# Kernel optimization log

Hardware: AMD Instinct MI355X
Metric: run time of the kernel (lower is better)

## Reference

```python
import jax, jax.numpy as jnp
import numpy as np

NQ = 8          # n_qubits
NC = 4          # n_cycles of the angle encoder
PI = np.float32(np.pi)
LAYER_QUBITS = [[0, 1, 2, 3, 4, 5, 6, 7], [1, 3, 5, 7]]  # active qubits per conv layer
FINAL_QUBITS = [3, 7]                                    # active after last pooling
CX = jnp.array([[1, 0, 0, 0], [0, 1, 0, 0], [0, 0, 0, 1], [0, 0, 1, 0]], jnp.complex64)


def apply1(psi, U, q):
    """Apply 1-qubit gate U ((2,2) shared or (B,2,2) batched) on qubit q. psi: (B,2,...,2)."""
    psi = jnp.moveaxis(psi, 1 + q, -1)
    if U.ndim == 3:
        psi = jnp.einsum('bij,b...j->b...i', U, psi)
    else:
        psi = jnp.einsum('ij,...j->...i', U, psi)
    return jnp.moveaxis(psi, -1, 1 + q)


def apply2(psi, U, q0, q1):
    """Apply 2-qubit gate U (4,4) on (q0,q1); q0 is the more-significant wire."""
    psi = jnp.moveaxis(psi, (1 + q0, 1 + q1), (-2, -1))
    sh = psi.shape
    psi = jnp.einsum('ij,...j->...i', U, psi.reshape(sh[:-2] + (4,)))
    return jnp.moveaxis(psi.reshape(sh), (-2, -1), (1 + q0, 1 + q1))


def rz_mat(t):
    return jnp.array([[jnp.exp(-0.5j * t), 0.0], [0.0, jnp.exp(0.5j * t)]]).astype(jnp.complex64)


def ry_mat(t):
    c, s = jnp.cos(t / 2), jnp.sin(t / 2)
    return jnp.array([[c, -s], [s, c]]).astype(jnp.complex64)


def crx_mat(t):
    c = jnp.cos(t / 2).astype(jnp.complex64)
    s = jnp.sin(t / 2).astype(jnp.complex64)
    M = jnp.eye(4, dtype=jnp.complex64)
    return M.at[2, 2].set(c).at[3, 3].set(c).at[2, 3].set(-1j * s).at[3, 2].set(-1j * s)


def u3_mat(t, p, l):
    c, s = jnp.cos(t / 2), jnp.sin(t / 2)
    return jnp.array([[c + 0j, -jnp.exp(1j * l) * s],
                      [jnp.exp(1j * p) * s, jnp.exp(1j * (p + l)) * c]]).astype(jnp.complex64)


def expz(psi, q):
    """<Z_q> = P(q=0) - P(q=1)."""
    p = psi.real ** 2 + psi.imag ** 2
    p = jnp.moveaxis(p, 1 + q, 1).reshape(p.shape[0], 2, -1).sum(-1)
    return p[:, 0] - p[:, 1]


def encode(x):
    """Angle-encoding circuit (circuit_builder): NC cycles of RY(x) + CNOT ring."""
    B = x.shape[0]
    psi = jnp.zeros((B, 2 ** NQ), jnp.complex64).at[:, 0].set(1.0).reshape((B,) + (2,) * NQ)
    for c in range(NC):
        ang = x[:, c * NQ:(c + 1) * NQ]
        cc, ss = jnp.cos(ang / 2), jnp.sin(ang / 2)
        for q in range(NQ):
            U = jnp.stack([jnp.stack([cc[:, q], -ss[:, q]], -1),
                           jnp.stack([ss[:, q], cc[:, q]], -1)], -2).astype(jnp.complex64)
            psi = apply1(psi, U, q)
        for q in range(NQ):
            psi = apply2(psi, CX, q, (q + 1) % NQ)
    return psi


def forward(x, rz_p, ry_p, ry2_p, crx_p, u3_p, u3b_p, W1, b1, W2, b2):
    psi0 = encode(x)
    psi1 = psi0  # deepcopy of encoded state for the second feature map
    for layer in range(2):
        aq = LAYER_QUBITS[layer]
        n = len(aq)
        RZp, RYp, RY2p = rz_mat(rz_p[layer]), ry_mat(ry_p[layer]), ry_mat(ry2_p[layer])
        RZm, RZpl = rz_mat(-PI / 2), rz_mat(PI / 2)
        # circuit 1: ZNOTY-style conv blocks, even pairs then odd pairs
        for parity in (0, 1):
            for i in range(parity, n - 1, 2):
                qc, qt = aq[i], aq[i + 1]
                psi0 = apply1(psi0, RZm, qt)
                psi0 = apply2(psi0, CX, qt, qc)
                psi0 = apply1(psi0, RZp, qc)
                psi0 = apply1(psi0, RYp, qt)
                psi0 = apply2(psi0, CX, qc, qt)
                psi0 = apply1(psi0, RY2p, qt)
                psi0 = apply2(psi0, CX, qt, qc)
                psi0 = apply1(psi0, RZpl, qc)
        remain = [aq[i] for i in range(n) if i % 2 == 1]
        U3a = u3_mat(u3_p[layer, 0], u3_p[layer, 1], u3_p[layer, 2])
        for q in remain:
            psi0 = apply1(psi0, U3a, q)
        # circuit 2: CRX conv blocks, even pairs then odd pairs
        CRXp = crx_mat(crx_p[layer])
        for parity in (0, 1):
            for i in range(parity, n - 1, 2):
                psi1 = apply2(psi1, CRXp, aq[i], aq[i + 1])
        U3b = u3_mat(u3b_p[layer, 0], u3b_p[layer, 1], u3b_p[layer, 2])
        for q in remain:
            psi1 = apply1(psi1, U3b, q)
    xv = jnp.stack([expz(psi0, q) for q in FINAL_QUBITS], 1)  # (B,2)
    yv = jnp.stack([expz(psi1, q) for q in FINAL_QUBITS], 1)  # (B,2)
    feat = jnp.concatenate([xv, yv], 1)                       # (B,4)
    h = jnp.tanh(feat @ W1.T + b1)
    return jax.nn.sigmoid(h @ W2.T + b2)


def setup_inputs() -> dict:
    key = jax.random.key(0)
    ks = jax.random.split(key, 12)
    B = 8192
    return {
        'x': jax.random.normal(ks[0], (B, NC * NQ), jnp.float32),
        'rz_p': jax.random.normal(ks[1], (2,), jnp.float32) * 0.5,
        'ry_p': jax.random.normal(ks[2], (2,), jnp.float32) * 0.5,
        'ry2_p': jax.random.normal(ks[3], (2,), jnp.float32) * 0.5,
        'crx_p': jax.random.normal(ks[4], (2,), jnp.float32) * 0.5,
        'u3_p': jax.random.normal(ks[5], (2, 3), jnp.float32) * 0.5,
        'u3b_p': jax.random.normal(ks[6], (2, 3), jnp.float32) * 0.5,
        'W1': jax.random.normal(ks[7], (15, 4), jnp.float32) * 0.4,
        'b1': jax.random.normal(ks[8], (15,), jnp.float32) * 0.1,
        'W2': jax.random.normal(ks[9], (1, 15), jnp.float32) * 0.25,
        'b2': jax.random.normal(ks[10], (1,), jnp.float32) * 0.1,
    }


def reference(x, rz_p, ry_p, ry2_p, crx_p, u3_p, u3b_p, W1, b1, W2, b2):
    return forward(x, rz_p, ry_p, ry2_p, crx_p, u3_p, u3b_p, W1, b1, W2, b2)
```

## Files before the change

kernel.cpp:

```cpp
#include <hip/hip_runtime.h>

#define DEV __device__ __forceinline__

struct C2 { float r, i; };


template<int P>
DEV void ry_cross(float* pr, float* pi, float gc, float gs, int lane) {
  const float cb = ((lane >> P) & 1) ? gs : -gs;
  #pragma unroll
  for (int s = 0; s < 16; ++s) {
    float br = __shfl_xor(pr[s], 1 << P);
    float bi = __shfl_xor(pi[s], 1 << P);
    pr[s] = gc * pr[s] + cb * br;
    pi[s] = gc * pi[s] + cb * bi;
  }
}

template<int M>
DEV void ry_in(float* pr, float* pi, float gc, float gs) {
  #pragma unroll
  for (int s = 0; s < 16; ++s) if (!(s & M)) {
    const int s1 = s | M;
    float ar = pr[s], ai = pi[s], br = pr[s1], bi = pi[s1];
    pr[s]  = gc * ar - gs * br;  pi[s]  = gc * ai - gs * bi;
    pr[s1] = gs * ar + gc * br;  pi[s1] = gs * ai + gc * bi;
  }
}

template<int PC, int PT>
DEV void cx_cc(float* pr, float* pi, int lane) {
  const bool h = (lane >> PC) & 1;
  #pragma unroll
  for (int s = 0; s < 16; ++s) {
    float tr = __shfl_xor(pr[s], 1 << PT);
    float ti = __shfl_xor(pi[s], 1 << PT);
    pr[s] = h ? tr : pr[s];
    pi[s] = h ? ti : pi[s];
  }
}

template<int PC, int MT>
DEV void cx_ci(float* pr, float* pi, int lane) {
  const bool h = (lane >> PC) & 1;
  #pragma unroll
  for (int s = 0; s < 16; ++s) if (!(s & MT)) {
    const int s1 = s | MT;
    float ar = pr[s], br = pr[s1];
    pr[s] = h ? br : ar;  pr[s1] = h ? ar : br;
    float ai = pi[s], bi = pi[s1];
    pi[s] = h ? bi : ai;  pi[s1] = h ? ai : bi;
  }
}

template<int MC, int MT>
DEV void cx_ii(float* pr, float* pi) {
  #pragma unroll
  for (int s = 0; s < 16; ++s) if ((s & MC) && !(s & MT)) {
    const int s1 = s | MT;
    float t;
    t = pr[s]; pr[s] = pr[s1]; pr[s1] = t;
    t = pi[s]; pi[s] = pi[s1]; pi[s1] = t;
  }
}

template<int MC, int PT>
DEV void cx_ic(float* pr, float* pi) {
  #pragma unroll
  for (int s = 0; s < 16; ++s) if (s & MC) {
    pr[s] = __shfl_xor(pr[s], 1 << PT);
    pi[s] = __shfl_xor(pi[s], 1 << PT);
  }
}


template<int PC, int PT>
DEV void u4_cc(float* pr, float* pi, const float* cw, int lay, int lane) {
  const int bc = (lane >> PC) & 1, bt = (lane >> PT) & 1;
  const int r = (bc << 1) | bt;
  const int base = (lay * 16 + r * 4) * 2;
  const float w0r = cw[base + (r ^ 0) * 2], w0i = cw[base + (r ^ 0) * 2 + 1];
  const float w1r = cw[base + (r ^ 1) * 2], w1i = cw[base + (r ^ 1) * 2 + 1];
  const float w2r = cw[base + (r ^ 2) * 2], w2i = cw[base + (r ^ 2) * 2 + 1];
  const float w3r = cw[base + (r ^ 3) * 2], w3i = cw[base + (r ^ 3) * 2 + 1];
  #pragma unroll
  for (int s = 0; s < 16; ++s) {
    float ar = pr[s], ai = pi[s];
    float tr = __shfl_xor(ar, 1 << PT), ti = __shfl_xor(ai, 1 << PT);
    float cr = __shfl_xor(ar, 1 << PC), ci = __shfl_xor(ai, 1 << PC);
    float ur = __shfl_xor(tr, 1 << PC), ui = __shfl_xor(ti, 1 << PC);
    pr[s] = w0r*ar - w0i*ai + w1r*tr - w1i*ti + w2r*cr - w2i*ci + w3r*ur - w3i*ui;
    pi[s] = w0r*ai + w0i*ar + w1r*ti + w1i*tr + w2r*ci + w2i*cr + w3r*ui + w3i*ur;
  }
}

template<int PC, int MT>
DEV void u4_ci(float* pr, float* pi, const float* cw, int lay, int lane) {
  const int bc = (lane >> PC) & 1;
  const int r0 = bc << 1, r1 = r0 | 1;
  const int b0 = (lay * 16 + r0 * 4) * 2;
  const int b1 = (lay * 16 + r1 * 4) * 2;
  const float A0r = cw[b0 + (r0 ^ 0) * 2], A0i = cw[b0 + (r0 ^ 0) * 2 + 1];
  const float A1r = cw[b0 + (r0 ^ 1) * 2], A1i = cw[b0 + (r0 ^ 1) * 2 + 1];
  const float A2r = cw[b0 + (r0 ^ 2) * 2], A2i = cw[b0 + (r0 ^ 2) * 2 + 1];
  const float A3r = cw[b0 + (r0 ^ 3) * 2], A3i = cw[b0 + (r0 ^ 3) * 2 + 1];
  const float B0r = cw[b1 + (r1 ^ 0) * 2], B0i = cw[b1 + (r1 ^ 0) * 2 + 1];
  const float B1r = cw[b1 + (r1 ^ 1) * 2], B1i = cw[b1 + (r1 ^ 1) * 2 + 1];
  const float B2r = cw[b1 + (r1 ^ 2) * 2], B2i = cw[b1 + (r1 ^ 2) * 2 + 1];
  const float B3r = cw[b1 + (r1 ^ 3) * 2], B3i = cw[b1 + (r1 ^ 3) * 2 + 1];
  #pragma unroll
  for (int s = 0; s < 16; ++s) if (!(s & MT)) {
    const int s1 = s | MT;
    float ar = pr[s], ai = pi[s], br = pr[s1], bi = pi[s1];
    float xar = __shfl_xor(ar, 1 << PC), xai = __shfl_xor(ai, 1 << PC);
    float xbr = __shfl_xor(br, 1 << PC), xbi = __shfl_xor(bi, 1 << PC);
    pr[s]  = A0r*ar - A0i*ai + A1r*br - A1i*bi + A2r*xar - A2i*xai + A3r*xbr - A3i*xbi;
    pi[s]  = A0r*ai + A0i*ar + A1r*bi + A1i*br + A2r*xai + A2i*xar + A3r*xbi + A3i*xbr;
    pr[s1] = B0r*br - B0i*bi + B1r*ar - B1i*ai + B2r*xbr - B2i*xbi + B3r*xar - B3i*xai;
    pi[s1] = B0r*bi + B0i*br + B1r*ai + B1i*ar + B2r*xbi + B2i*xbr + B3r*xai + B3i*xar;
  }
}

template<int MC, int MT>
DEV void u4_ii(float* pr, float* pi, const float* cw, int lay) {
  float u[32];
  #pragma unroll
  for (int k = 0; k < 32; ++k) u[k] = cw[lay * 32 + k];
  #pragma unroll
  for (int s = 0; s < 16; ++s) if (!(s & (MC | MT))) {
    const int s0 = s, s1 = s | MT, s2 = s | MC, s3 = s | MC | MT;
    float v0r = pr[s0], v0i = pi[s0], v1r = pr[s1], v1i = pi[s1];
    float v2r = pr[s2], v2i = pi[s2], v3r = pr[s3], v3i = pi[s3];
    float n0r = u[0]*v0r - u[1]*v0i + u[2]*v1r - u[3]*v1i + u[4]*v2r - u[5]*v2i + u[6]*v3r - u[7]*v3i;
    float n0i = u[0]*v0i + u[1]*v0r + u[2]*v1i + u[3]*v1r + u[4]*v2i + u[5]*v2r + u[6]*v3i + u[7]*v3r;
    float n1r = u[8]*v0r - u[9]*v0i + u[10]*v1r - u[11]*v1i + u[12]*v2r - u[13]*v2i + u[14]*v3r - u[15]*v3i;
    float n1i = u[8]*v0i + u[9]*v0r + u[10]*v1i + u[11]*v1r + u[12]*v2i + u[13]*v2r + u[14]*v3i + u[15]*v3r;
    float n2r = u[16]*v0r - u[17]*v0i + u[18]*v1r - u[19]*v1i + u[20]*v2r - u[21]*v2i + u[22]*v3r - u[23]*v3i;
    float n2i = u[16]*v0i + u[17]*v0r + u[18]*v1i + u[19]*v1r + u[20]*v2i + u[21]*v2r + u[22]*v3i + u[23]*v3r;
    float n3r = u[24]*v0r - u[25]*v0i + u[26]*v1r - u[27]*v1i + u[28]*v2r - u[29]*v2i + u[30]*v3r - u[31]*v3i;
    float n3i = u[24]*v0i + u[25]*v0r + u[26]*v1i + u[27]*v1r + u[28]*v2i + u[29]*v2r + u[30]*v3i + u[31]*v3r;
    pr[s0] = n0r; pi[s0] = n0i; pr[s1] = n1r; pi[s1] = n1i;
    pr[s2] = n2r; pi[s2] = n2i; pr[s3] = n3r; pi[s3] = n3i;
  }
}


DEV void u3_make(float t, float p, float l, C2* u) {
  float c = __cosf(0.5f * t), s = __sinf(0.5f * t);
  float cp = __cosf(p), sp = __sinf(p);
  float cl = __cosf(l), sl = __sinf(l);
  float cpl = __cosf(p + l), spl = __sinf(p + l);
  u[0] = C2{c, 0.0f};
  u[1] = C2{-cl * s, -sl * s};
  u[2] = C2{cp * s, sp * s};
  u[3] = C2{cpl * c, spl * c};
}

template<int P>
DEV void u3_cross(float* pr, float* pi, const C2* u, int lane) {
  const bool h = (lane >> P) & 1;
  const float car = h ? u[3].r : u[0].r, cai = h ? u[3].i : u[0].i;
  const float cbr = h ? u[2].r : u[1].r, cbi = h ? u[2].i : u[1].i;
  #pragma unroll
  for (int s = 0; s < 16; ++s) {
    float br = __shfl_xor(pr[s], 1 << P);
    float bi = __shfl_xor(pi[s], 1 << P);
    float ar = pr[s], ai = pi[s];
    pr[s] = car*ar - cai*ai + cbr*br - cbi*bi;
    pi[s] = car*ai + cai*ar + cbr*bi + cbi*br;
  }
}

template<int M>
DEV void u3_in(float* pr, float* pi, const C2* u) {
  #pragma unroll
  for (int s = 0; s < 16; ++s) if (!(s & M)) {
    const int s1 = s | M;
    float ar = pr[s], ai = pi[s], br = pr[s1], bi = pi[s1];
    pr[s]  = u[0].r*ar - u[0].i*ai + u[1].r*br - u[1].i*bi;
    pi[s]  = u[0].r*ai + u[0].i*ar + u[1].r*bi + u[1].i*br;
    pr[s1] = u[2].r*ar - u[2].i*ai + u[3].r*br - u[3].i*bi;
    pi[s1] = u[2].r*ai + u[2].i*ar + u[3].r*bi + u[3].i*br;
  }
}


template<int PC, int PT>
DEV void crx_cc(float* pr, float* pi, float c, float s, int lane) {
  const bool h = (lane >> PC) & 1;
  const float cc = h ? c : 1.0f;
  const float ss = h ? s : 0.0f;
  #pragma unroll
  for (int k = 0; k < 16; ++k) {
    float br = __shfl_xor(pr[k], 1 << PT);
    float bi = __shfl_xor(pi[k], 1 << PT);
    float ar = pr[k], ai = pi[k];
    pr[k] = cc * ar + ss * bi;
    pi[k] = cc * ai - ss * br;
  }
}

template<int PC, int MT>
DEV void crx_ci(float* pr, float* pi, float c, float s, int lane) {
  const bool h = (lane >> PC) & 1;
  const float cc = h ? c : 1.0f;
  const float ss = h ? s : 0.0f;
  #pragma unroll
  for (int k = 0; k < 16; ++k) if (!(k & MT)) {
    const int k1 = k | MT;
    float ar = pr[k], ai = pi[k], br = pr[k1], bi = pi[k1];
    pr[k]  = cc * ar + ss * bi;
    pi[k]  = cc * ai - ss * br;
    pr[k1] = cc * br + ss * ai;
    pi[k1] = cc * bi - ss * ar;
  }
}

template<int MC, int MT>
DEV void crx_ii(float* pr, float* pi, float c, float s) {
  #pragma unroll
  for (int k = 0; k < 16; ++k) if ((k & MC) && !(k & MT)) {
    const int k1 = k | MT;
    float ar = pr[k], ai = pi[k], br = pr[k1], bi = pi[k1];
    pr[k]  = c * ar + s * bi;
    pi[k]  = c * ai - s * br;
    pr[k1] = c * br + s * ai;
    pi[k1] = c * bi - s * ar;
  }
}


DEV void expz37(const float* pr, const float* pi, int lane, float& z3, float& z7) {
  float t3 = 0.0f, t7 = 0.0f;
  #pragma unroll
  for (int s = 0; s < 16; ++s) {
    float p = pr[s] * pr[s] + pi[s] * pi[s];
    t3 += p;
    t7 += (s & 1) ? -p : p;
  }
  t3 = (lane & 1) ? -t3 : t3;
  #pragma unroll
  for (int m = 1; m < 16; m <<= 1) {
    t3 += __shfl_xor(t3, m);
    t7 += __shfl_xor(t7, m);
  }
  z3 = t3; z7 = t7;
}


__global__ __launch_bounds__(256, 2)
void qcnn_kernel(const float* __restrict__ x,
                 const float* __restrict__ rz_p, const float* __restrict__ ry_p,
                 const float* __restrict__ ry2_p, const float* __restrict__ crx_p,
                 const float* __restrict__ u3_p, const float* __restrict__ u3b_p,
                 const float* __restrict__ W1, const float* __restrict__ b1,
                 const float* __restrict__ W2, const float* __restrict__ b2,
                 float* __restrict__ out, int B) {
  __shared__ float cw[64];

  const int tid  = threadIdx.x;
  const int lane = tid & 63;
  const int wave = tid >> 6;
  const int grp  = lane >> 4;
  const int sub  = lane & 15;
  const int elem = blockIdx.x * 16 + wave * 4 + grp;
  const int elemc = elem < B ? elem : (B - 1);

  if (lane < 32) {
    const int lay = lane >> 4, e = lane & 15, i4 = e >> 2, j4 = e & 3;
    const int base = lane & 48;
    const float c45 = 0.70710678118654752f;
    float rz = rz_p[lay], ry = ry_p[lay], ry2 = ry2_p[lay];
    float mr = (i4 == j4) ? c45 : 0.0f;
    float mi = (i4 == j4) ? ((i4 & 1) ? -c45 : c45) : 0.0f;
    { int t = (i4 & 1) ? (i4 ^ 2) : i4; int src = base | (t << 2) | j4;
      mr = __shfl(mr, src); mi = __shfl(mi, src); }
    { float cz = __cosf(0.5f * rz), sz = __sinf(0.5f * rz);
      float di = (i4 & 2) ? sz : -sz;
      float nr = cz * mr - di * mi, ni = cz * mi + di * mr; mr = nr; mi = ni; }
    { float cy = __cosf(0.5f * ry), sy = __sinf(0.5f * ry);
      int src = base | ((i4 ^ 1) << 2) | j4;
      float orr = __shfl(mr, src), oii = __shfl(mi, src);
      float sg = (i4 & 1) ? sy : -sy;
      mr = cy * mr + sg * orr; mi = cy * mi + sg * oii; }
    { int t = (i4 & 2) ? (i4 ^ 1) : i4; int src = base | (t << 2) | j4;
      mr = __shfl(mr, src); mi = __shfl(mi, src); }
    { float cy = __cosf(0.5f * ry2), sy = __sinf(0.5f * ry2);
      int src = base | ((i4 ^ 1) << 2) | j4;
      float orr = __shfl(mr, src), oii = __shfl(mi, src);
      float sg = (i4 & 1) ? sy : -sy;
      mr = cy * mr + sg * orr; mi = cy * mi + sg * oii; }
    { int t = (i4 & 1) ? (i4 ^ 2) : i4; int src = base | (t << 2) | j4;
      mr = __shfl(mr, src); mi = __shfl(mi, src); }
    { float di = (i4 & 2) ? c45 : -c45;
      float nr = c45 * mr - di * mi, ni = c45 * mi + di * mr; mr = nr; mi = ni; }
    cw[(lay * 16 + e) * 2]     = mr;
    cw[(lay * 16 + e) * 2 + 1] = mi;
  }

  float2 aa = ((const float2*)x)[(size_t)elemc * 16 + sub];
  float ch0 = __cosf(0.5f * aa.x), sh0 = __sinf(0.5f * aa.x);
  float ch1 = __cosf(0.5f * aa.y), sh1 = __sinf(0.5f * aa.y);

  float pr[16], pi[16];
  #pragma unroll
  for (int s = 0; s < 16; ++s) { pr[s] = 0.0f; pi[s] = 0.0f; }
  pr[0] = (sub == 0) ? 1.0f : 0.0f;

  #pragma unroll 1
  for (int c = 0; c < 4; ++c) {
    const int sb = lane & 48;
    float gc, gs;
    gc = __shfl(ch0, sb | (c * 4 + 0)); gs = __shfl(sh0, sb | (c * 4 + 0));
    ry_cross<3>(pr, pi, gc, gs, lane);
    gc = __shfl(ch1, sb | (c * 4 + 0)); gs = __shfl(sh1, sb | (c * 4 + 0));
    ry_cross<2>(pr, pi, gc, gs, lane);
    gc = __shfl(ch0, sb | (c * 4 + 1)); gs = __shfl(sh0, sb | (c * 4 + 1));
    ry_cross<1>(pr, pi, gc, gs, lane);
    gc = __shfl(ch1, sb | (c * 4 + 1)); gs = __shfl(sh1, sb | (c * 4 + 1));
    ry_cross<0>(pr, pi, gc, gs, lane);
    gc = __shfl(ch0, sb | (c * 4 + 2)); gs = __shfl(sh0, sb | (c * 4 + 2));
    ry_in<8>(pr, pi, gc, gs);
    gc = __shfl(ch1, sb | (c * 4 + 2)); gs = __shfl(sh1, sb | (c * 4 + 2));
    ry_in<4>(pr, pi, gc, gs);
    gc = __shfl(ch0, sb | (c * 4 + 3)); gs = __shfl(sh0, sb | (c * 4 + 3));
    ry_in<2>(pr, pi, gc, gs);
    gc = __shfl(ch1, sb | (c * 4 + 3)); gs = __shfl(sh1, sb | (c * 4 + 3));
    ry_in<1>(pr, pi, gc, gs);
    cx_cc<3, 2>(pr, pi, lane);
    cx_cc<2, 1>(pr, pi, lane);
    cx_cc<1, 0>(pr, pi, lane);
    cx_ci<0, 8>(pr, pi, lane);
    cx_ii<8, 4>(pr, pi);
    cx_ii<4, 2>(pr, pi);
    cx_ii<2, 1>(pr, pi);
    cx_ic<1, 3>(pr, pi);
  }

  float qr[16], qi[16];
  #pragma unroll
  for (int s = 0; s < 16; ++s) { qr[s] = pr[s]; qi[s] = pi[s]; }

  __syncthreads();

  u4_cc<3, 2>(pr, pi, cw, 0, lane);
  u4_cc<1, 0>(pr, pi, cw, 0, lane);
  u4_ii<8, 4>(pr, pi, cw, 0);
  u4_ii<2, 1>(pr, pi, cw, 0);
  u4_cc<2, 1>(pr, pi, cw, 0, lane);
  u4_ci<0, 8>(pr, pi, cw, 0, lane);
  u4_ii<4, 2>(pr, pi, cw, 0);
  {
    C2 u[4]; u3_make(u3_p[0], u3_p[1], u3_p[2], u);
    u3_cross<2>(pr, pi, u, lane);
    u3_cross<0>(pr, pi, u, lane);
    u3_in<4>(pr, pi, u);
    u3_in<1>(pr, pi, u);
  }
  u4_cc<2, 0>(pr, pi, cw, 1, lane);
  u4_ii<4, 1>(pr, pi, cw, 1);
  u4_ci<0, 4>(pr, pi, cw, 1, lane);
  {
    C2 u[4]; u3_make(u3_p[3], u3_p[4], u3_p[5], u);
    u3_cross<0>(pr, pi, u, lane);
    u3_in<1>(pr, pi, u);
  }

  {
    float t = crx_p[0];
    float cc = __cosf(0.5f * t), ss = __sinf(0.5f * t);
    crx_cc<3, 2>(qr, qi, cc, ss, lane);
    crx_cc<1, 0>(qr, qi, cc, ss, lane);
    crx_ii<8, 4>(qr, qi, cc, ss);
    crx_ii<2, 1>(qr, qi, cc, ss);
    crx_cc<2, 1>(qr, qi, cc, ss, lane);
    crx_ci<0, 8>(qr, qi, cc, ss, lane);
    crx_ii<4, 2>(qr, qi, cc, ss);
  }
  {
    C2 u[4]; u3_make(u3b_p[0], u3b_p[1], u3b_p[2], u);
    u3_cross<2>(qr, qi, u, lane);
    u3_cross<0>(qr, qi, u, lane);
    u3_in<4>(qr, qi, u);
    u3_in<1>(qr, qi, u);
  }
  {
    float t = crx_p[1];
    float cc = __cosf(0.5f * t), ss = __sinf(0.5f * t);
    crx_cc<2, 0>(qr, qi, cc, ss, lane);
    crx_ii<4, 1>(qr, qi, cc, ss);
    crx_ci<0, 4>(qr, qi, cc, ss, lane);
  }
  {
    C2 u[4]; u3_make(u3b_p[3], u3b_p[4], u3b_p[5], u);
    u3_cross<0>(qr, qi, u, lane);
    u3_in<1>(qr, qi, u);
  }

  float f0, f1, f2, f3;
  expz37(pr, pi, lane, f0, f1);
  expz37(qr, qi, lane, f2, f3);

  const int j = (sub < 15) ? sub : 0;
  float acc = W1[j * 4 + 0] * f0 + W1[j * 4 + 1] * f1 +
              W1[j * 4 + 2] * f2 + W1[j * 4 + 3] * f3 + b1[j];
  float e2 = __expf(2.0f * acc);
  float th = (e2 - 1.0f) / (e2 + 1.0f);
  float part = (sub < 15) ? th * W2[j] : 0.0f;
  #pragma unroll
  for (int m = 1; m < 16; m <<= 1) part += __shfl_xor(part, m);

  if (sub == 0 && elem < B) {
    float z = part + b2[0];
    out[elem] = 1.0f / (1.0f + __expf(-z));
  }
}

extern "C" void kernel_launch(void* const* d_in, const int* in_sizes, int n_in,
                              void* d_out, int out_size, void* d_ws, size_t ws_size,
                              hipStream_t stream) {
  (void)n_in; (void)out_size; (void)d_ws; (void)ws_size;
  const float* x     = (const float*)d_in[0];
  const float* rz_p  = (const float*)d_in[1];
  const float* ry_p  = (const float*)d_in[2];
  const float* ry2_p = (const float*)d_in[3];
  const float* crx_p = (const float*)d_in[4];
  const float* u3_p  = (const float*)d_in[5];
  const float* u3b_p = (const float*)d_in[6];
  const float* W1    = (const float*)d_in[7];
  const float* b1    = (const float*)d_in[8];
  const float* W2    = (const float*)d_in[9];
  const float* b2    = (const float*)d_in[10];
  float* out = (float*)d_out;

  const int B = in_sizes[0] / 32;
  const int blocks = (B + 15) / 16;
  qcnn_kernel<<<dim3(blocks), dim3(256), 0, stream>>>(
      x, rz_p, ry_p, ry2_p, crx_p, u3_p, u3b_p, W1, b1, W2, b2, out, B);
}
```

Measured before the change: 133.1 us.

## Map each batch element's 256-amplitude state to a full wavefront

Each state vector is now spread across a full 64-lane wave with 4 amplitudes per lane, instead of 16 lanes with 16 amplitudes each. All gate helpers are remapped so most qubits become cross-lane shuffles, and a dense 4x4 in-register gate is added. Blocks now handle 4 elements instead of 16, and the launch bound asks for more resident blocks. The aim is to cut register pressure and raise occupancy, at the cost of many more cross-lane shuffles per gate.

```diff
diff --git a/kernel.cpp b/kernel.cpp
--- a/kernel.cpp
+++ b/kernel.cpp
@@ -9,7 +9,7 @@
 DEV void ry_cross(float* pr, float* pi, float gc, float gs, int lane) {
   const float cb = ((lane >> P) & 1) ? gs : -gs;
   #pragma unroll
-  for (int s = 0; s < 16; ++s) {
+  for (int s = 0; s < 4; ++s) {
     float br = __shfl_xor(pr[s], 1 << P);
     float bi = __shfl_xor(pi[s], 1 << P);
     pr[s] = gc * pr[s] + cb * br;
@@ -20,7 +20,7 @@
 template<int M>
 DEV void ry_in(float* pr, float* pi, float gc, float gs) {
   #pragma unroll
-  for (int s = 0; s < 16; ++s) if (!(s & M)) {
+  for (int s = 0; s < 4; ++s) if (!(s & M)) {
     const int s1 = s | M;
     float ar = pr[s], ai = pi[s], br = pr[s1], bi = pi[s1];
     pr[s]  = gc * ar - gs * br;  pi[s]  = gc * ai - gs * bi;
@@ -32,7 +32,7 @@
 DEV void cx_cc(float* pr, float* pi, int lane) {
   const bool h = (lane >> PC) & 1;
   #pragma unroll
-  for (int s = 0; s < 16; ++s) {
+  for (int s = 0; s < 4; ++s) {
     float tr = __shfl_xor(pr[s], 1 << PT);
     float ti = __shfl_xor(pi[s], 1 << PT);
     pr[s] = h ? tr : pr[s];
@@ -44,7 +44,7 @@
 DEV void cx_ci(float* pr, float* pi, int lane) {
   const bool h = (lane >> PC) & 1;
   #pragma unroll
-  for (int s = 0; s < 16; ++s) if (!(s & MT)) {
+  for (int s = 0; s < 4; ++s) if (!(s & MT)) {
     const int s1 = s | MT;
     float ar = pr[s], br = pr[s1];
     pr[s] = h ? br : ar;  pr[s1] = h ? ar : br;
@@ -56,7 +56,7 @@
 template<int MC, int MT>
 DEV void cx_ii(float* pr, float* pi) {
   #pragma unroll
-  for (int s = 0; s < 16; ++s) if ((s & MC) && !(s & MT)) {
+  for (int s = 0; s < 4; ++s) if ((s & MC) && !(s & MT)) {
     const int s1 = s | MT;
     float t;
     t = pr[s]; pr[s] = pr[s1]; pr[s1] = t;
@@ -67,7 +67,7 @@
 template<int MC, int PT>
 DEV void cx_ic(float* pr, float* pi) {
   #pragma unroll
-  for (int s = 0; s < 16; ++s) if (s & MC) {
+  for (int s = 0; s < 4; ++s) if (s & MC) {
     pr[s] = __shfl_xor(pr[s], 1 << PT);
     pi[s] = __shfl_xor(pi[s], 1 << PT);
   }
@@ -76,19 +76,18 @@
 
 template<int PC, int PT>
 DEV void u4_cc(float* pr, float* pi, const float* cw, int lay, int lane) {
-  const int bc = (lane >> PC) & 1, bt = (lane >> PT) & 1;
-  const int r = (bc << 1) | bt;
+  const int r = (((lane >> PC) & 1) << 1) | ((lane >> PT) & 1);
   const int base = (lay * 16 + r * 4) * 2;
   const float w0r = cw[base + (r ^ 0) * 2], w0i = cw[base + (r ^ 0) * 2 + 1];
   const float w1r = cw[base + (r ^ 1) * 2], w1i = cw[base + (r ^ 1) * 2 + 1];
   const float w2r = cw[base + (r ^ 2) * 2], w2i = cw[base + (r ^ 2) * 2 + 1];
   const float w3r = cw[base + (r ^ 3) * 2], w3i = cw[base + (r ^ 3) * 2 + 1];
   #pragma unroll
-  for (int s = 0; s < 16; ++s) {
+  for (int s = 0; s < 4; ++s) {
     float ar = pr[s], ai = pi[s];
-    float tr = __shfl_xor(ar, 1 << PT), ti = __shfl_xor(ai, 1 << PT);
-    float cr = __shfl_xor(ar, 1 << PC), ci = __shfl_xor(ai, 1 << PC);
-    float ur = __shfl_xor(tr, 1 << PC), ui = __shfl_xor(ti, 1 << PC);
+    float tr = __shfl_xor(ar, 1 << PT),              ti = __shfl_xor(ai, 1 << PT);
+    float cr = __shfl_xor(ar, 1 << PC),              ci = __shfl_xor(ai, 1 << PC);
+    float ur = __shfl_xor(ar, (1 << PC) | (1 << PT)), ui = __shfl_xor(ai, (1 << PC) | (1 << PT));
     pr[s] = w0r*ar - w0i*ai + w1r*tr - w1i*ti + w2r*cr - w2i*ci + w3r*ur - w3i*ui;
     pi[s] = w0r*ai + w0i*ar + w1r*ti + w1i*tr + w2r*ci + w2i*cr + w3r*ui + w3i*ur;
   }
@@ -109,7 +108,7 @@
   const float B2r = cw[b1 + (r1 ^ 2) * 2], B2i = cw[b1 + (r1 ^ 2) * 2 + 1];
   const float B3r = cw[b1 + (r1 ^ 3) * 2], B3i = cw[b1 + (r1 ^ 3) * 2 + 1];
   #pragma unroll
-  for (int s = 0; s < 16; ++s) if (!(s & MT)) {
+  for (int s = 0; s < 4; ++s) if (!(s & MT)) {
     const int s1 = s | MT;
     float ar = pr[s], ai = pi[s], br = pr[s1], bi = pi[s1];
     float xar = __shfl_xor(ar, 1 << PC), xai = __shfl_xor(ai, 1 << PC);
@@ -121,27 +120,22 @@
   }
 }
 
-template<int MC, int MT>
-DEV void u4_ii(float* pr, float* pi, const float* cw, int lay) {
-  float u[32];
-  #pragma unroll
-  for (int k = 0; k < 32; ++k) u[k] = cw[lay * 32 + k];
-  #pragma unroll
-  for (int s = 0; s < 16; ++s) if (!(s & (MC | MT))) {
-    const int s0 = s, s1 = s | MT, s2 = s | MC, s3 = s | MC | MT;
-    float v0r = pr[s0], v0i = pi[s0], v1r = pr[s1], v1i = pi[s1];
-    float v2r = pr[s2], v2i = pi[s2], v3r = pr[s3], v3i = pi[s3];
-    float n0r = u[0]*v0r - u[1]*v0i + u[2]*v1r - u[3]*v1i + u[4]*v2r - u[5]*v2i + u[6]*v3r - u[7]*v3i;
-    float n0i = u[0]*v0i + u[1]*v0r + u[2]*v1i + u[3]*v1r + u[4]*v2i + u[5]*v2r + u[6]*v3i + u[7]*v3r;
-    float n1r = u[8]*v0r - u[9]*v0i + u[10]*v1r - u[11]*v1i + u[12]*v2r - u[13]*v2i + u[14]*v3r - u[15]*v3i;
-    float n1i = u[8]*v0i + u[9]*v0r + u[10]*v1i + u[11]*v1r + u[12]*v2i + u[13]*v2r + u[14]*v3i + u[15]*v3r;
-    float n2r = u[16]*v0r - u[17]*v0i + u[18]*v1r - u[19]*v1i + u[20]*v2r - u[21]*v2i + u[22]*v3r - u[23]*v3i;
-    float n2i = u[16]*v0i + u[17]*v0r + u[18]*v1i + u[19]*v1r + u[20]*v2i + u[21]*v2r + u[22]*v3i + u[23]*v3r;
-    float n3r = u[24]*v0r - u[25]*v0i + u[26]*v1r - u[27]*v1i + u[28]*v2r - u[29]*v2i + u[30]*v3r - u[31]*v3i;
-    float n3i = u[24]*v0i + u[25]*v0r + u[26]*v1i + u[27]*v1r + u[28]*v2i + u[29]*v2r + u[30]*v3i + u[31]*v3r;
-    pr[s0] = n0r; pi[s0] = n0i; pr[s1] = n1r; pi[s1] = n1i;
-    pr[s2] = n2r; pi[s2] = n2i; pr[s3] = n3r; pi[s3] = n3i;
-  }
+DEV void u4_ii_full(float* pr, float* pi, const float* cw, int lay) {
+  float nr[4], ni[4];
+  #pragma unroll
+  for (int r = 0; r < 4; ++r) {
+    float ar = 0.0f, ai = 0.0f;
+    #pragma unroll
+    for (int c = 0; c < 4; ++c) {
+      float ur = cw[(lay * 16 + r * 4 + c) * 2];
+      float ui = cw[(lay * 16 + r * 4 + c) * 2 + 1];
+      ar += ur * pr[c] - ui * pi[c];
+      ai += ur * pi[c] + ui * pr[c];
+    }
+    nr[r] = ar; ni[r] = ai;
+  }
+  #pragma unroll
+  for (int r = 0; r < 4; ++r) { pr[r] = nr[r]; pi[r] = ni[r]; }
 }
 
 
@@ -162,7 +156,7 @@
   const float car = h ? u[3].r : u[0].r, cai = h ? u[3].i : u[0].i;
   const float cbr = h ? u[2].r : u[1].r, cbi = h ? u[2].i : u[1].i;
   #pragma unroll
-  for (int s = 0; s < 16; ++s) {
+  for (int s = 0; s < 4; ++s) {
     float br = __shfl_xor(pr[s], 1 << P);
     float bi = __shfl_xor(pi[s], 1 << P);
     float ar = pr[s], ai = pi[s];
@@ -174,7 +168,7 @@
 template<int M>
 DEV void u3_in(float* pr, float* pi, const C2* u) {
   #pragma unroll
-  for (int s = 0; s < 16; ++s) if (!(s & M)) {
+  for (int s = 0; s < 4; ++s) if (!(s & M)) {
     const int s1 = s | M;
     float ar = pr[s], ai = pi[s], br = pr[s1], bi = pi[s1];
     pr[s]  = u[0].r*ar - u[0].i*ai + u[1].r*br - u[1].i*bi;
@@ -191,7 +185,7 @@
   const float cc = h ? c : 1.0f;
   const float ss = h ? s : 0.0f;
   #pragma unroll
-  for (int k = 0; k < 16; ++k) {
+  for (int k = 0; k < 4; ++k) {
     float br = __shfl_xor(pr[k], 1 << PT);
     float bi = __shfl_xor(pi[k], 1 << PT);
     float ar = pr[k], ai = pi[k];
@@ -206,7 +200,7 @@
   const float cc = h ? c : 1.0f;
   const float ss = h ? s : 0.0f;
   #pragma unroll
-  for (int k = 0; k < 16; ++k) if (!(k & MT)) {
+  for (int k = 0; k < 4; ++k) if (!(k & MT)) {
     const int k1 = k | MT;
     float ar = pr[k], ai = pi[k], br = pr[k1], bi = pi[k1];
     pr[k]  = cc * ar + ss * bi;
@@ -219,7 +213,7 @@
 template<int MC, int MT>
 DEV void crx_ii(float* pr, float* pi, float c, float s) {
   #pragma unroll
-  for (int k = 0; k < 16; ++k) if ((k & MC) && !(k & MT)) {
+  for (int k = 0; k < 4; ++k) if ((k & MC) && !(k & MT)) {
     const int k1 = k | MT;
     float ar = pr[k], ai = pi[k], br = pr[k1], bi = pi[k1];
     pr[k]  = c * ar + s * bi;
@@ -233,14 +227,14 @@
 DEV void expz37(const float* pr, const float* pi, int lane, float& z3, float& z7) {
   float t3 = 0.0f, t7 = 0.0f;
   #pragma unroll
-  for (int s = 0; s < 16; ++s) {
+  for (int s = 0; s < 4; ++s) {
     float p = pr[s] * pr[s] + pi[s] * pi[s];
     t3 += p;
     t7 += (s & 1) ? -p : p;
   }
-  t3 = (lane & 1) ? -t3 : t3;
-  #pragma unroll
-  for (int m = 1; m < 16; m <<= 1) {
+  t3 = ((lane >> 2) & 1) ? -t3 : t3;
+  #pragma unroll
+  for (int m = 1; m < 64; m <<= 1) {
     t3 += __shfl_xor(t3, m);
     t7 += __shfl_xor(t7, m);
   }
@@ -248,7 +242,7 @@
 }
 
 
-__global__ __launch_bounds__(256, 2)
+__global__ __launch_bounds__(256, 8)
 void qcnn_kernel(const float* __restrict__ x,
                  const float* __restrict__ rz_p, const float* __restrict__ ry_p,
                  const float* __restrict__ ry2_p, const float* __restrict__ crx_p,
@@ -261,14 +255,12 @@
   const int tid  = threadIdx.x;
   const int lane = tid & 63;
   const int wave = tid >> 6;
-  const int grp  = lane >> 4;
-  const int sub  = lane & 15;
-  const int elem = blockIdx.x * 16 + wave * 4 + grp;
+  const int elem = blockIdx.x * 4 + wave;
   const int elemc = elem < B ? elem : (B - 1);
 
-  if (lane < 32) {
-    const int lay = lane >> 4, e = lane & 15, i4 = e >> 2, j4 = e & 3;
-    const int base = lane & 48;
+  if (tid < 32) {
+    const int lay = tid >> 4, e = tid & 15, i4 = e >> 2, j4 = e & 3;
+    const int base = tid & 48;
     const float c45 = 0.70710678118654752f;
     float rz = rz_p[lay], ry = ry_p[lay], ry2 = ry2_p[lay];
     float mr = (i4 == j4) ? c45 : 0.0f;
@@ -298,102 +290,93 @@
     cw[(lay * 16 + e) * 2 + 1] = mi;
   }
 
-  float2 aa = ((const float2*)x)[(size_t)elemc * 16 + sub];
-  float ch0 = __cosf(0.5f * aa.x), sh0 = __sinf(0.5f * aa.x);
-  float ch1 = __cosf(0.5f * aa.y), sh1 = __sinf(0.5f * aa.y);
-
-  float pr[16], pi[16];
-  #pragma unroll
-  for (int s = 0; s < 16; ++s) { pr[s] = 0.0f; pi[s] = 0.0f; }
-  pr[0] = (sub == 0) ? 1.0f : 0.0f;
+  float a0 = x[(size_t)elemc * 32 + (lane & 31)];
+  float ch = __cosf(0.5f * a0), sh = __sinf(0.5f * a0);
+
+  float pr[4], pi[4];
+  #pragma unroll
+  for (int s = 0; s < 4; ++s) { pr[s] = 0.0f; pi[s] = 0.0f; }
+  pr[0] = (lane == 0) ? 1.0f : 0.0f;
 
   #pragma unroll 1
   for (int c = 0; c < 4; ++c) {
-    const int sb = lane & 48;
+    const int cb = c * 8;
     float gc, gs;
-    gc = __shfl(ch0, sb | (c * 4 + 0)); gs = __shfl(sh0, sb | (c * 4 + 0));
-    ry_cross<3>(pr, pi, gc, gs, lane);
-    gc = __shfl(ch1, sb | (c * 4 + 0)); gs = __shfl(sh1, sb | (c * 4 + 0));
-    ry_cross<2>(pr, pi, gc, gs, lane);
-    gc = __shfl(ch0, sb | (c * 4 + 1)); gs = __shfl(sh0, sb | (c * 4 + 1));
-    ry_cross<1>(pr, pi, gc, gs, lane);
-    gc = __shfl(ch1, sb | (c * 4 + 1)); gs = __shfl(sh1, sb | (c * 4 + 1));
-    ry_cross<0>(pr, pi, gc, gs, lane);
-    gc = __shfl(ch0, sb | (c * 4 + 2)); gs = __shfl(sh0, sb | (c * 4 + 2));
-    ry_in<8>(pr, pi, gc, gs);
-    gc = __shfl(ch1, sb | (c * 4 + 2)); gs = __shfl(sh1, sb | (c * 4 + 2));
-    ry_in<4>(pr, pi, gc, gs);
-    gc = __shfl(ch0, sb | (c * 4 + 3)); gs = __shfl(sh0, sb | (c * 4 + 3));
-    ry_in<2>(pr, pi, gc, gs);
-    gc = __shfl(ch1, sb | (c * 4 + 3)); gs = __shfl(sh1, sb | (c * 4 + 3));
-    ry_in<1>(pr, pi, gc, gs);
+    gc = __shfl(ch, cb + 0); gs = __shfl(sh, cb + 0); ry_cross<5>(pr, pi, gc, gs, lane);
+    gc = __shfl(ch, cb + 1); gs = __shfl(sh, cb + 1); ry_cross<4>(pr, pi, gc, gs, lane);
+    gc = __shfl(ch, cb + 2); gs = __shfl(sh, cb + 2); ry_cross<3>(pr, pi, gc, gs, lane);
+    gc = __shfl(ch, cb + 3); gs = __shfl(sh, cb + 3); ry_cross<2>(pr, pi, gc, gs, lane);
+    gc = __shfl(ch, cb + 4); gs = __shfl(sh, cb + 4); ry_cross<1>(pr, pi, gc, gs, lane);
+    gc = __shfl(ch, cb + 5); gs = __shfl(sh, cb + 5); ry_cross<0>(pr, pi, gc, gs, lane);
+    gc = __shfl(ch, cb + 6); gs = __shfl(sh, cb + 6); ry_in<2>(pr, pi, gc, gs);
+    gc = __shfl(ch, cb + 7); gs = __shfl(sh, cb + 7); ry_in<1>(pr, pi, gc, gs);
+    cx_cc<5, 4>(pr, pi, lane);
+    cx_cc<4, 3>(pr, pi, lane);
     cx_cc<3, 2>(pr, pi, lane);
     cx_cc<2, 1>(pr, pi, lane);
     cx_cc<1, 0>(pr, pi, lane);
-    cx_ci<0, 8>(pr, pi, lane);
-    cx_ii<8, 4>(pr, pi);
-    cx_ii<4, 2>(pr, pi);
+    cx_ci<0, 2>(pr, pi, lane);
     cx_ii<2, 1>(pr, pi);
-    cx_ic<1, 3>(pr, pi);
-  }
-
-  float qr[16], qi[16];
-  #pragma unroll
-  for (int s = 0; s < 16; ++s) { qr[s] = pr[s]; qi[s] = pi[s]; }
+    cx_ic<1, 5>(pr, pi);
+  }
+
+  float qr[4], qi[4];
+  #pragma unroll
+  for (int s = 0; s < 4; ++s) { qr[s] = pr[s]; qi[s] = pi[s]; }
 
   __syncthreads();
 
+  u4_cc<5, 4>(pr, pi, cw, 0, lane);
   u4_cc<3, 2>(pr, pi, cw, 0, lane);
   u4_cc<1, 0>(pr, pi, cw, 0, lane);
-  u4_ii<8, 4>(pr, pi, cw, 0);
-  u4_ii<2, 1>(pr, pi, cw, 0);
+  u4_ii_full(pr, pi, cw, 0);
+  u4_cc<4, 3>(pr, pi, cw, 0, lane);
   u4_cc<2, 1>(pr, pi, cw, 0, lane);
-  u4_ci<0, 8>(pr, pi, cw, 0, lane);
-  u4_ii<4, 2>(pr, pi, cw, 0);
+  u4_ci<0, 2>(pr, pi, cw, 0, lane);
   {
     C2 u[4]; u3_make(u3_p[0], u3_p[1], u3_p[2], u);
+    u3_cross<4>(pr, pi, u, lane);
     u3_cross<2>(pr, pi, u, lane);
     u3_cross<0>(pr, pi, u, lane);
-    u3_in<4>(pr, pi, u);
     u3_in<1>(pr, pi, u);
   }
+  u4_cc<4, 2>(pr, pi, cw, 1, lane);
+  u4_ci<0, 1>(pr, pi, cw, 1, lane);
   u4_cc<2, 0>(pr, pi, cw, 1, lane);
-  u4_ii<4, 1>(pr, pi, cw, 1);
-  u4_ci<0, 4>(pr, pi, cw, 1, lane);
   {
     C2 u[4]; u3_make(u3_p[3], u3_p[4], u3_p[5], u);
-    u3_cross<0>(pr, pi, u, lane);
+    u3_cross<2>(pr, pi, u, lane);
     u3_in<1>(pr, pi, u);
   }
 
   {
     float t = crx_p[0];
     float cc = __cosf(0.5f * t), ss = __sinf(0.5f * t);
+    crx_cc<5, 4>(qr, qi, cc, ss, lane);
     crx_cc<3, 2>(qr, qi, cc, ss, lane);
     crx_cc<1, 0>(qr, qi, cc, ss, lane);
-    crx_ii<8, 4>(qr, qi, cc, ss);
     crx_ii<2, 1>(qr, qi, cc, ss);
+    crx_cc<4, 3>(qr, qi, cc, ss, lane);
     crx_cc<2, 1>(qr, qi, cc, ss, lane);
-    crx_ci<0, 8>(qr, qi, cc, ss, lane);
-    crx_ii<4, 2>(qr, qi, cc, ss);
+    crx_ci<0, 2>(qr, qi, cc, ss, lane);
   }
   {
     C2 u[4]; u3_make(u3b_p[0], u3b_p[1], u3b_p[2], u);
+    u3_cross<4>(qr, qi, u, lane);
     u3_cross<2>(qr, qi, u, lane);
     u3_cross<0>(qr, qi, u, lane);
-    u3_in<4>(qr, qi, u);
     u3_in<1>(qr, qi, u);
   }
   {
     float t = crx_p[1];
     float cc = __cosf(0.5f * t), ss = __sinf(0.5f * t);
+    crx_cc<4, 2>(qr, qi, cc, ss, lane);
+    crx_ci<0, 1>(qr, qi, cc, ss, lane);
     crx_cc<2, 0>(qr, qi, cc, ss, lane);
-    crx_ii<4, 1>(qr, qi, cc, ss);
-    crx_ci<0, 4>(qr, qi, cc, ss, lane);
   }
   {
     C2 u[4]; u3_make(u3b_p[3], u3b_p[4], u3b_p[5], u);
-    u3_cross<0>(qr, qi, u, lane);
+    u3_cross<2>(qr, qi, u, lane);
     u3_in<1>(qr, qi, u);
   }
 
@@ -401,6 +384,7 @@
   expz37(pr, pi, lane, f0, f1);
   expz37(qr, qi, lane, f2, f3);
 
+  const int sub = lane & 15;
   const int j = (sub < 15) ? sub : 0;
   float acc = W1[j * 4 + 0] * f0 + W1[j * 4 + 1] * f1 +
               W1[j * 4 + 2] * f2 + W1[j * 4 + 3] * f3 + b1[j];
@@ -410,7 +394,7 @@
   #pragma unroll
   for (int m = 1; m < 16; m <<= 1) part += __shfl_xor(part, m);
 
-  if (sub == 0 && elem < B) {
+  if (lane == 0 && elem < B) {
     float z = part + b2[0];
     out[elem] = 1.0f / (1.0f + __expf(-z));
   }
@@ -434,7 +418,7 @@
   float* out = (float*)d_out;
 
   const int B = in_sizes[0] / 32;
-  const int blocks = (B + 15) / 16;
+  const int blocks = (B + 3) / 4;
   qcnn_kernel<<<dim3(blocks), dim3(256), 0, stream>>>(
       x, rz_p, ry_p, ry2_p, crx_p, u3_p, u3b_p, W1, b1, W2, b2, out, B);
 }
```

Measured after the change: 151.7 us. 1.14x slower.
